# Performance work log

Hardware: AMD Instinct MI355X
Metric: run time of the kernel (lower is better)

The kernel has to match this reference:

```python
import jax, jax.numpy as jnp
import numpy as np

B, T, D = 8, 2048, 256
Q, K = 8, 1024


def setup_inputs() -> dict:
    key = jax.random.key(0)
    k1, k2 = jax.random.split(key)
    x = jax.random.normal(k1, (B, T, D), dtype=jnp.float32)
    codebooks = jax.random.normal(k2, (Q, K, D), dtype=jnp.float32)
    return {"x": x, "codebooks": codebooks}


def _vq_layer(residual, codebook):
    # residual: [B, T, D], codebook: [K, D]
    b, t, d = residual.shape
    flat = residual.reshape(-1, d)                      # [N, D]
    dist = (2.0 * flat @ codebook.T
            - jnp.sum(flat * flat, axis=-1, keepdims=True)
            - jnp.sum(codebook * codebook, axis=-1))    # [N, K]
    idx = jnp.argmax(dist, axis=-1)                     # [N]
    quantize = codebook[idx].reshape(b, t, d)           # gather
    # commitment loss (codebook updated via EMA in torch, not gradient)
    loss = jnp.mean((jax.lax.stop_gradient(quantize) - residual) ** 2)
    # straight-through estimator
    quantize_st = residual + jax.lax.stop_gradient(quantize - residual)
    return quantize_st, idx.reshape(b, t), loss


def reference(x, codebooks):
    def step(residual, codebook):
        q, idx, loss = _vq_layer(residual, codebook)
        return residual - q, (q, idx, loss)

    _, (qs, all_indices, all_losses) = jax.lax.scan(step, x, codebooks)
    quantized_out = jnp.sum(qs, axis=0)                 # [B, T, D]
    return quantized_out, all_indices, all_losses
```

## Files before the change

### kernel.cpp

```cpp
#include <hip/hip_runtime.h>


typedef _Float16 f16;
typedef f16 f16x8 __attribute__((ext_vector_type(8)));
typedef float f32x16 __attribute__((ext_vector_type(16)));

constexpr int Dd = 256;
constexpr int Kk = 1024;
constexpr int Qq = 8;
constexpr int Nn = 16384;

__device__ inline void gload16(const f16* g, f16* l) {
    __builtin_amdgcn_global_load_lds(
        (const __attribute__((address_space(1))) unsigned int*)(const __attribute__((address_space(1))) f16*)g,
        (__attribute__((address_space(3))) unsigned int*)(__attribute__((address_space(3))) f16*)l,
        16, 0, 0);
}

__global__ __launch_bounds__(256) void build_ecat(const float* __restrict__ cb,
                                                  f16* __restrict__ ecat,
                                                  float* __restrict__ norms) {
    int row = blockIdx.x * 8 + (threadIdx.x >> 5);
    int p = threadIdx.x & 31;
    const float* s = cb + (size_t)row * Dd + p * 8;
    f16x8 hi, lo;
    float sq = 0.f;
#pragma unroll
    for (int j = 0; j < 8; ++j) {
        float v = s[j];
        f16 h = (f16)v;
        hi[j] = h; lo[j] = (f16)(v - (float)h);
        sq = fmaf(v, v, sq);
    }
    *(f16x8*)(ecat + (size_t)row * 512 + p * 8) = hi;
    *(f16x8*)(ecat + (size_t)row * 512 + 256 + p * 8) = lo;
#pragma unroll
    for (int off = 16; off >= 1; off >>= 1) sq += __shfl_down(sq, off, 32);
    if (p == 0) norms[row] = sq;
}

__global__ __launch_bounds__(512, 2) void rvq_kernel(
    const float* __restrict__ x,
    const float* __restrict__ cbs,
    const f16* __restrict__ ecat,
    const float* __restrict__ norms,
    float* __restrict__ outq,
    float* __restrict__ idxs,
    float* __restrict__ losses)
{
    __shared__ f16 sA[2][16384];
    __shared__ f16 sB[32768];
    __shared__ float smn[1024];
    __shared__ float2 smg[4][64];
    __shared__ int bestk[64];
    __shared__ float lred[8];

    const int tid = threadIdx.x;
    const int w = tid >> 6, l = tid & 63;
    const int l32 = l & 31, lh = l >> 5;
    const int wcq = w >> 1;
    const int wt = w & 1;
    const int tbase = blockIdx.x * 64;
    const int ut = tid >> 3, ud = tid & 7;
    const int grow = tbase + ut;

    const int srow = tid >> 2;
    const int g = ((tid & 3) ^ ((tid >> 5) & 3)) * 8;

    int offA_[2][2];
#pragma unroll
    for (int m = 0; m < 2; ++m)
#pragma unroll
        for (int kh = 0; kh < 2; ++kh) {
            int row = wcq * 64 + m * 32 + l32;
            offA_[m][kh] = row * 32 + (((kh * 2 + lh) ^ ((row >> 3) & 3)) * 8);
        }
    int rbh[4][2];
#pragma unroll
    for (int cc = 0; cc < 4; ++cc)
#pragma unroll
        for (int kh = 0; kh < 2; ++kh) {
            int row = wt * 32 + l32;
            rbh[cc][kh] = row * 32 + ((((kh * 2 + lh) ^ ((row >> 3) & 3)) ^ cc) * 8);
        }

    float r[32];

#define STAGE(P, pp, c) do { \
        const f16* ga_ = gqs + (size_t)(pp) * 131072 + (c) * 32; \
        gload16(ga_,                  &sA[P][tid * 8]); \
        gload16(ga_ + 128 * 512,      &sA[P][4096 + tid * 8]); \
        gload16(ga_ + 256,            &sA[P][8192 + tid * 8]); \
        gload16(ga_ + 256 + 128 * 512,&sA[P][12288 + tid * 8]); \
    } while (0)

#pragma unroll 1
    for (int q = 0; q < Qq; ++q) {
        const f16* gqs = ecat + ((size_t)q * Kk + srow) * 512 + g;
        STAGE(0, 0, 0);
        STAGE(1, 0, 1);

        float lp = 0.f;
        if (q == 0) {
            const float4* xs = (const float4*)(x + (size_t)grow * Dd + ud * 32);
#pragma unroll
            for (int jv = 0; jv < 8; ++jv) {
                float4 v = xs[jv];
                r[jv * 4 + 0] = v.x; r[jv * 4 + 1] = v.y;
                r[jv * 4 + 2] = v.z; r[jv * 4 + 3] = v.w;
            }
        } else {
            const int k = bestk[ut];
            const float4* e4 = (const float4*)(cbs + ((size_t)(q - 1) * Kk + k) * Dd + ud * 32);
#pragma unroll
            for (int jv = 0; jv < 8; ++jv) {
                float4 v = e4[jv];
                r[jv * 4 + 0] -= v.x; r[jv * 4 + 1] -= v.y;
                r[jv * 4 + 2] -= v.z; r[jv * 4 + 3] -= v.w;
            }
#pragma unroll
            for (int j = 0; j < 32; ++j) lp = fmaf(r[j], r[j], lp);
            if ((tid & 7) == 0) idxs[(size_t)(q - 1) * Nn + grow] = (float)k;
#pragma unroll
            for (int off = 32; off >= 1; off >>= 1) lp += __shfl_down(lp, off);
            if (l == 0) lred[w] = lp;
        }
        {
            const int s = (ut >> 3) & 3;
#pragma unroll
            for (int qd = 0; qd < 4; ++qd) {
                f16x8 hi, lo;
#pragma unroll
                for (int j2 = 0; j2 < 8; ++j2) {
                    float v = 2.f * r[qd * 8 + j2];
                    f16 h = (f16)v;
                    hi[j2] = h; lo[j2] = (f16)(v - (float)h);
                }
                int a = ud * 2048 + ut * 32 + ((((qd ^ s) ^ (ud & 3)) & 3) * 8);
                *(f16x8*)&sB[a] = hi;
                *(f16x8*)&sB[16384 + a] = lo;
            }
        }
        smn[tid] = norms[q * Kk + tid];
        smn[512 + tid] = norms[q * Kk + 512 + tid];
        __syncthreads();
        if (q > 0 && tid == 0) {
            float s2 = 0.f;
#pragma unroll
            for (int i = 0; i < 8; ++i) s2 += lred[i];
            atomicAdd(losses + q - 1, s2 * (1.0f / ((float)Nn * (float)Dd)));
        }

        float bv = -3.4e38f; int bi = 0;
#pragma unroll 1
        for (int p = 0; p < 4; ++p) {
            f32x16 acc[2] = {};
#pragma unroll
            for (int c = 0; c < 8; ++c) {
                const int P = c & 1;
                if (c >= 1 && c < 7) STAGE(P ^ 1, p, c + 1);
#pragma unroll
                for (int kh = 0; kh < 2; ++kh) {
                    f16x8 a0 = *(const f16x8*)&sA[P][offA_[0][kh]];
                    f16x8 a1 = *(const f16x8*)&sA[P][offA_[1][kh]];
                    f16x8 bh = *(const f16x8*)&sB[c * 2048 + rbh[c & 3][kh]];
                    f16x8 bl = *(const f16x8*)&sB[16384 + c * 2048 + rbh[c & 3][kh]];
                    __builtin_amdgcn_s_setprio(1);
                    acc[0] = __builtin_amdgcn_mfma_f32_32x32x16_f16(a0, bh, acc[0], 0, 0, 0);
                    acc[1] = __builtin_amdgcn_mfma_f32_32x32x16_f16(a1, bh, acc[1], 0, 0, 0);
                    acc[0] = __builtin_amdgcn_mfma_f32_32x32x16_f16(a0, bl, acc[0], 0, 0, 0);
                    acc[1] = __builtin_amdgcn_mfma_f32_32x32x16_f16(a1, bl, acc[1], 0, 0, 0);
                    __builtin_amdgcn_s_setprio(0);
                    f16x8 e0 = *(const f16x8*)&sA[P][8192 + offA_[0][kh]];
                    f16x8 e1 = *(const f16x8*)&sA[P][8192 + offA_[1][kh]];
                    __builtin_amdgcn_s_setprio(1);
                    acc[0] = __builtin_amdgcn_mfma_f32_32x32x16_f16(e0, bh, acc[0], 0, 0, 0);
                    acc[1] = __builtin_amdgcn_mfma_f32_32x32x16_f16(e1, bh, acc[1], 0, 0, 0);
                    __builtin_amdgcn_s_setprio(0);
                }
                if (c < 7)
                    asm volatile("s_waitcnt vmcnt(0)\n\ts_barrier" ::: "memory");
            }
            asm volatile("s_barrier" ::: "memory");
            if (p < 3) { STAGE(0, p + 1, 0); STAGE(1, p + 1, 1); }
#pragma unroll
            for (int m = 0; m < 2; ++m) {
#pragma unroll
                for (int rr = 0; rr < 16; ++rr) {
                    int cl = wcq * 64 + m * 32 + (rr & 3) + 8 * (rr >> 2) + 4 * lh;
                    float v = acc[m][rr] - smn[p * 256 + cl];
                    int cg = p * 256 + cl;
                    if (v > bv) { bv = v; bi = cg; }
                }
            }
            if (p < 3)
                asm volatile("s_waitcnt vmcnt(4)\n\ts_barrier" ::: "memory");
        }
        {
            float ov = __shfl_xor(bv, 32);
            int oi = __shfl_xor(bi, 32);
            if (ov > bv || (ov == bv && oi < bi)) { bv = ov; bi = oi; }
            if (l < 32) smg[wcq][wt * 32 + l] = make_float2(bv, (float)bi);
            __syncthreads();
            if (tid < 64) {
                float2 r2 = smg[0][tid];
#pragma unroll
                for (int ww = 1; ww < 4; ++ww) {
                    float2 c2 = smg[ww][tid];
                    if (c2.x > r2.x || (c2.x == r2.x && c2.y < r2.y)) r2 = c2;
                }
                bestk[tid] = (int)r2.y;
            }
            __syncthreads();
        }
    }
#undef STAGE

    {
        const int k = bestk[ut];
        const float4* e4 = (const float4*)(cbs + ((size_t)7 * Kk + k) * Dd + ud * 32);
        float lp = 0.f;
#pragma unroll
        for (int jv = 0; jv < 8; ++jv) {
            float4 v = e4[jv];
            r[jv * 4 + 0] -= v.x; r[jv * 4 + 1] -= v.y;
            r[jv * 4 + 2] -= v.z; r[jv * 4 + 3] -= v.w;
        }
#pragma unroll
        for (int j = 0; j < 32; ++j) lp = fmaf(r[j], r[j], lp);
        const float4* xs = (const float4*)(x + (size_t)grow * Dd + ud * 32);
        float4* os = (float4*)(outq + (size_t)grow * Dd + ud * 32);
#pragma unroll
        for (int jv = 0; jv < 8; ++jv) {
            float4 xv = xs[jv];
            float4 o;
            o.x = xv.x - r[jv * 4 + 0]; o.y = xv.y - r[jv * 4 + 1];
            o.z = xv.z - r[jv * 4 + 2]; o.w = xv.w - r[jv * 4 + 3];
            os[jv] = o;
        }
        if ((tid & 7) == 0) idxs[(size_t)7 * Nn + grow] = (float)k;
#pragma unroll
        for (int off = 32; off >= 1; off >>= 1) lp += __shfl_down(lp, off);
        if (l == 0) lred[w] = lp;
        __syncthreads();
        if (tid == 0) {
            float s2 = 0.f;
#pragma unroll
            for (int i = 0; i < 8; ++i) s2 += lred[i];
            atomicAdd(losses + 7, s2 * (1.0f / ((float)Nn * (float)Dd)));
        }
    }
}

extern "C" void kernel_launch(void* const* d_in, const int* in_sizes, int n_in,
                              void* d_out, int out_size, void* d_ws, size_t ws_size,
                              hipStream_t stream) {
    const float* x   = (const float*)d_in[0];
    const float* cbs = (const float*)d_in[1];
    float* out    = (float*)d_out;
    float* idxs   = out + (size_t)Nn * Dd;
    float* losses = idxs + (size_t)Qq * Nn;

    f16* ecat    = (f16*)d_ws;
    float* norms = (float*)(ecat + (size_t)Qq * Kk * 512);

    hipMemsetAsync(losses, 0, Qq * sizeof(float), stream);
    build_ecat<<<(Qq * Kk) / 8, 256, 0, stream>>>(cbs, ecat, norms);
    rvq_kernel<<<Nn / 64, 512, 0, stream>>>(x, cbs, ecat, norms,
                                            out, idxs, losses);
}
```

Baseline: 284.8 us.

## Load codebook MFMA fragments directly from global into registers, drop LDS staging

Removes the double-buffered LDS staging of the fp16 hi/lo codebook tiles (global_load_lds plus per-chunk barriers). Each wave now reads its A fragments straight from global memory into registers, with a one-step register prefetch. This is meant to cut barrier synchronisation and LDS traffic and pressure. In exchange, codebook rows that were shared through LDS are now fetched by each wave separately, relying on L1/L2 caching. Global-load latency is now exposed, hidden only by a shallow prefetch.

New measurement: 518.7 us. 82.1% more time.

```diff
diff --git a/kernel.cpp b/kernel.cpp
--- a/kernel.cpp
+++ b/kernel.cpp
@@ -9,13 +9,6 @@
 constexpr int Kk = 1024;
 constexpr int Qq = 8;
 constexpr int Nn = 16384;
-
-__device__ inline void gload16(const f16* g, f16* l) {
-    __builtin_amdgcn_global_load_lds(
-        (const __attribute__((address_space(1))) unsigned int*)(const __attribute__((address_space(1))) f16*)g,
-        (__attribute__((address_space(3))) unsigned int*)(__attribute__((address_space(3))) f16*)l,
-        16, 0, 0);
-}
 
 __global__ __launch_bounds__(256) void build_ecat(const float* __restrict__ cb,
                                                   f16* __restrict__ ecat,
@@ -48,7 +41,6 @@
     float* __restrict__ idxs,
     float* __restrict__ losses)
 {
-    __shared__ f16 sA[2][16384];
     __shared__ f16 sB[32768];
     __shared__ float smn[1024];
     __shared__ float2 smg[4][64];
@@ -64,17 +56,6 @@
     const int ut = tid >> 3, ud = tid & 7;
     const int grow = tbase + ut;
 
-    const int srow = tid >> 2;
-    const int g = ((tid & 3) ^ ((tid >> 5) & 3)) * 8;
-
-    int offA_[2][2];
-#pragma unroll
-    for (int m = 0; m < 2; ++m)
-#pragma unroll
-        for (int kh = 0; kh < 2; ++kh) {
-            int row = wcq * 64 + m * 32 + l32;
-            offA_[m][kh] = row * 32 + (((kh * 2 + lh) ^ ((row >> 3) & 3)) * 8);
-        }
     int rbh[4][2];
 #pragma unroll
     for (int cc = 0; cc < 4; ++cc)
@@ -86,20 +67,8 @@
 
     float r[32];
 
-#define STAGE(P, pp, c) do { \
-        const f16* ga_ = gqs + (size_t)(pp) * 131072 + (c) * 32; \
-        gload16(ga_,                  &sA[P][tid * 8]); \
-        gload16(ga_ + 128 * 512,      &sA[P][4096 + tid * 8]); \
-        gload16(ga_ + 256,            &sA[P][8192 + tid * 8]); \
-        gload16(ga_ + 256 + 128 * 512,&sA[P][12288 + tid * 8]); \
-    } while (0)
-
 #pragma unroll 1
     for (int q = 0; q < Qq; ++q) {
-        const f16* gqs = ecat + ((size_t)q * Kk + srow) * 512 + g;
-        STAGE(0, 0, 0);
-        STAGE(1, 0, 1);
-
         float lp = 0.f;
         if (q == 0) {
             const float4* xs = (const float4*)(x + (size_t)grow * Dd + ud * 32);
@@ -154,35 +123,39 @@
         float bv = -3.4e38f; int bi = 0;
 #pragma unroll 1
         for (int p = 0; p < 4; ++p) {
+            const f16* a0p = ecat + ((size_t)q * Kk + p * 256 + wcq * 64 + l32) * 512 + lh * 8;
+            const f16* a1p = a0p + (size_t)32 * 512;
+
             f32x16 acc[2] = {};
-#pragma unroll
-            for (int c = 0; c < 8; ++c) {
-                const int P = c & 1;
-                if (c >= 1 && c < 7) STAGE(P ^ 1, p, c + 1);
-#pragma unroll
-                for (int kh = 0; kh < 2; ++kh) {
-                    f16x8 a0 = *(const f16x8*)&sA[P][offA_[0][kh]];
-                    f16x8 a1 = *(const f16x8*)&sA[P][offA_[1][kh]];
-                    f16x8 bh = *(const f16x8*)&sB[c * 2048 + rbh[c & 3][kh]];
-                    f16x8 bl = *(const f16x8*)&sB[16384 + c * 2048 + rbh[c & 3][kh]];
-                    __builtin_amdgcn_s_setprio(1);
-                    acc[0] = __builtin_amdgcn_mfma_f32_32x32x16_f16(a0, bh, acc[0], 0, 0, 0);
-                    acc[1] = __builtin_amdgcn_mfma_f32_32x32x16_f16(a1, bh, acc[1], 0, 0, 0);
-                    acc[0] = __builtin_amdgcn_mfma_f32_32x32x16_f16(a0, bl, acc[0], 0, 0, 0);
-                    acc[1] = __builtin_amdgcn_mfma_f32_32x32x16_f16(a1, bl, acc[1], 0, 0, 0);
-                    __builtin_amdgcn_s_setprio(0);
-                    f16x8 e0 = *(const f16x8*)&sA[P][8192 + offA_[0][kh]];
-                    f16x8 e1 = *(const f16x8*)&sA[P][8192 + offA_[1][kh]];
-                    __builtin_amdgcn_s_setprio(1);
-                    acc[0] = __builtin_amdgcn_mfma_f32_32x32x16_f16(e0, bh, acc[0], 0, 0, 0);
-                    acc[1] = __builtin_amdgcn_mfma_f32_32x32x16_f16(e1, bh, acc[1], 0, 0, 0);
-                    __builtin_amdgcn_s_setprio(0);
-                }
-                if (c < 7)
-                    asm volatile("s_waitcnt vmcnt(0)\n\ts_barrier" ::: "memory");
-            }
-            asm volatile("s_barrier" ::: "memory");
-            if (p < 3) { STAGE(0, p + 1, 0); STAGE(1, p + 1, 1); }
+            f16x8 fa0[2], fa1[2], fe0[2], fe1[2], fbh[2], fbl[2];
+
+#define LOADF(S, IDX) do { \
+            const int c_ = (IDX) >> 1, kh_ = (IDX) & 1; \
+            const int co_ = c_ * 32 + kh_ * 16; \
+            fa0[S] = *(const f16x8*)(a0p + co_); \
+            fa1[S] = *(const f16x8*)(a1p + co_); \
+            fe0[S] = *(const f16x8*)(a0p + 256 + co_); \
+            fe1[S] = *(const f16x8*)(a1p + 256 + co_); \
+            fbh[S] = *(const f16x8*)&sB[c_ * 2048 + rbh[c_ & 3][kh_]]; \
+            fbl[S] = *(const f16x8*)&sB[16384 + c_ * 2048 + rbh[c_ & 3][kh_]]; \
+        } while (0)
+
+            LOADF(0, 0);
+#pragma unroll
+            for (int idx = 0; idx < 16; ++idx) {
+                const int cur = idx & 1;
+                if (idx < 15) LOADF(cur ^ 1, idx + 1);
+                __builtin_amdgcn_s_setprio(1);
+                acc[0] = __builtin_amdgcn_mfma_f32_32x32x16_f16(fa0[cur], fbh[cur], acc[0], 0, 0, 0);
+                acc[1] = __builtin_amdgcn_mfma_f32_32x32x16_f16(fa1[cur], fbh[cur], acc[1], 0, 0, 0);
+                acc[0] = __builtin_amdgcn_mfma_f32_32x32x16_f16(fa0[cur], fbl[cur], acc[0], 0, 0, 0);
+                acc[1] = __builtin_amdgcn_mfma_f32_32x32x16_f16(fa1[cur], fbl[cur], acc[1], 0, 0, 0);
+                acc[0] = __builtin_amdgcn_mfma_f32_32x32x16_f16(fe0[cur], fbh[cur], acc[0], 0, 0, 0);
+                acc[1] = __builtin_amdgcn_mfma_f32_32x32x16_f16(fe1[cur], fbh[cur], acc[1], 0, 0, 0);
+                __builtin_amdgcn_s_setprio(0);
+            }
+#undef LOADF
+
 #pragma unroll
             for (int m = 0; m < 2; ++m) {
 #pragma unroll
@@ -193,8 +166,6 @@
                     if (v > bv) { bv = v; bi = cg; }
                 }
             }
-            if (p < 3)
-                asm volatile("s_waitcnt vmcnt(4)\n\ts_barrier" ::: "memory");
         }
         {
             float ov = __shfl_xor(bv, 32);
@@ -214,7 +185,6 @@
             __syncthreads();
         }
     }
-#undef STAGE
 
     {
         const int k = bestk[ut];
```

## Double block to 1024 threads covering 512 codewords per pass with finer K-chunk staging

Applied to the files above, without the earlier changes.

The RVQ kernel now launches 1024 threads (16 waves) per block, so each pass covers 512 codebook rows instead of 256 and two passes replace four. The A-tile staging is restructured into 16 half-chunks of 16 columns with one hi/lo load pair per thread, and double-buffering runs continuously across the pass boundary. Each thread holds 16 residual elements instead of 32, which lowers register pressure. The aim is more waves in flight to hide load latency and fewer pass-boundary stalls, at the cost of a barrier every half-chunk across 16 waves and a launch bound that may force register spills.

Result: slower. 334.4 us (+17.4%).

```diff
diff --git a/kernel.cpp b/kernel.cpp
--- a/kernel.cpp
+++ b/kernel.cpp
@@ -39,7 +39,7 @@
     if (p == 0) norms[row] = sq;
 }
 
-__global__ __launch_bounds__(512, 2) void rvq_kernel(
+__global__ __launch_bounds__(1024, 4) void rvq_kernel(
     const float* __restrict__ x,
     const float* __restrict__ cbs,
     const f16* __restrict__ ecat,
@@ -51,30 +51,25 @@
     __shared__ f16 sA[2][16384];
     __shared__ f16 sB[32768];
     __shared__ float smn[1024];
-    __shared__ float2 smg[4][64];
+    __shared__ float2 smg[8][64];
     __shared__ int bestk[64];
-    __shared__ float lred[8];
+    __shared__ float lred[16];
 
     const int tid = threadIdx.x;
     const int w = tid >> 6, l = tid & 63;
     const int l32 = l & 31, lh = l >> 5;
-    const int wcq = w >> 1;
+    const int cs = w >> 1;
     const int wt = w & 1;
     const int tbase = blockIdx.x * 64;
-    const int ut = tid >> 3, ud = tid & 7;
+    const int ut = tid >> 4, h = tid & 15;
     const int grow = tbase + ut;
 
-    const int srow = tid >> 2;
-    const int g = ((tid & 3) ^ ((tid >> 5) & 3)) * 8;
-
-    int offA_[2][2];
-#pragma unroll
-    for (int m = 0; m < 2; ++m)
-#pragma unroll
-        for (int kh = 0; kh < 2; ++kh) {
-            int row = wcq * 64 + m * 32 + l32;
-            offA_[m][kh] = row * 32 + (((kh * 2 + lh) ^ ((row >> 3) & 3)) * 8);
-        }
+    int offA[2];
+#pragma unroll
+    for (int m = 0; m < 2; ++m) {
+        int ra = cs * 64 + m * 32 + l32;
+        offA[m] = ra * 16 + ((lh ^ ((ra >> 2) & 1)) * 8);
+    }
     int rbh[4][2];
 #pragma unroll
     for (int cc = 0; cc < 4; ++cc)
@@ -84,128 +79,120 @@
             rbh[cc][kh] = row * 32 + ((((kh * 2 + lh) ^ ((row >> 3) & 3)) ^ cc) * 8);
         }
 
-    float r[32];
-
-#define STAGE(P, pp, c) do { \
-        const f16* ga_ = gqs + (size_t)(pp) * 131072 + (c) * 32; \
-        gload16(ga_,                  &sA[P][tid * 8]); \
-        gload16(ga_ + 128 * 512,      &sA[P][4096 + tid * 8]); \
-        gload16(ga_ + 256,            &sA[P][8192 + tid * 8]); \
-        gload16(ga_ + 256 + 128 * 512,&sA[P][12288 + tid * 8]); \
+    const int ch8 = (((tid & 1) ^ ((tid >> 3) & 1))) * 8;
+
+    float r[16];
+
+#define STAGE(P, PP, HC) do { \
+        const f16* ga_ = ecat + ((size_t)q * Kk + (PP) * 512 + (tid >> 1)) * 512 + (HC) * 16 + ch8; \
+        gload16(ga_,       &sA[P][tid * 8]); \
+        gload16(ga_ + 256, &sA[P][8192 + tid * 8]); \
     } while (0)
 
 #pragma unroll 1
     for (int q = 0; q < Qq; ++q) {
-        const f16* gqs = ecat + ((size_t)q * Kk + srow) * 512 + g;
         STAGE(0, 0, 0);
-        STAGE(1, 0, 1);
 
         float lp = 0.f;
         if (q == 0) {
-            const float4* xs = (const float4*)(x + (size_t)grow * Dd + ud * 32);
-#pragma unroll
-            for (int jv = 0; jv < 8; ++jv) {
+            const float4* xs = (const float4*)(x + (size_t)grow * Dd + h * 16);
+#pragma unroll
+            for (int jv = 0; jv < 4; ++jv) {
                 float4 v = xs[jv];
                 r[jv * 4 + 0] = v.x; r[jv * 4 + 1] = v.y;
                 r[jv * 4 + 2] = v.z; r[jv * 4 + 3] = v.w;
             }
         } else {
             const int k = bestk[ut];
-            const float4* e4 = (const float4*)(cbs + ((size_t)(q - 1) * Kk + k) * Dd + ud * 32);
-#pragma unroll
-            for (int jv = 0; jv < 8; ++jv) {
+            const float4* e4 = (const float4*)(cbs + ((size_t)(q - 1) * Kk + k) * Dd + h * 16);
+#pragma unroll
+            for (int jv = 0; jv < 4; ++jv) {
                 float4 v = e4[jv];
                 r[jv * 4 + 0] -= v.x; r[jv * 4 + 1] -= v.y;
                 r[jv * 4 + 2] -= v.z; r[jv * 4 + 3] -= v.w;
             }
 #pragma unroll
-            for (int j = 0; j < 32; ++j) lp = fmaf(r[j], r[j], lp);
-            if ((tid & 7) == 0) idxs[(size_t)(q - 1) * Nn + grow] = (float)k;
+            for (int j = 0; j < 16; ++j) lp = fmaf(r[j], r[j], lp);
+            if (h == 0) idxs[(size_t)(q - 1) * Nn + grow] = (float)k;
 #pragma unroll
             for (int off = 32; off >= 1; off >>= 1) lp += __shfl_down(lp, off);
             if (l == 0) lred[w] = lp;
         }
         {
             const int s = (ut >> 3) & 3;
-#pragma unroll
-            for (int qd = 0; qd < 4; ++qd) {
+            const int st = h >> 1;
+#pragma unroll
+            for (int j = 0; j < 2; ++j) {
+                const int qq = (h & 1) * 2 + j;
                 f16x8 hi, lo;
 #pragma unroll
                 for (int j2 = 0; j2 < 8; ++j2) {
-                    float v = 2.f * r[qd * 8 + j2];
-                    f16 h = (f16)v;
-                    hi[j2] = h; lo[j2] = (f16)(v - (float)h);
+                    float v = 2.f * r[j * 8 + j2];
+                    f16 hv = (f16)v;
+                    hi[j2] = hv; lo[j2] = (f16)(v - (float)hv);
                 }
-                int a = ud * 2048 + ut * 32 + ((((qd ^ s) ^ (ud & 3)) & 3) * 8);
+                int a = st * 2048 + ut * 32 + (((qq ^ s) ^ (st & 3)) & 3) * 8;
                 *(f16x8*)&sB[a] = hi;
                 *(f16x8*)&sB[16384 + a] = lo;
             }
         }
         smn[tid] = norms[q * Kk + tid];
-        smn[512 + tid] = norms[q * Kk + 512 + tid];
         __syncthreads();
         if (q > 0 && tid == 0) {
             float s2 = 0.f;
 #pragma unroll
-            for (int i = 0; i < 8; ++i) s2 += lred[i];
+            for (int i = 0; i < 16; ++i) s2 += lred[i];
             atomicAdd(losses + q - 1, s2 * (1.0f / ((float)Nn * (float)Dd)));
         }
 
         float bv = -3.4e38f; int bi = 0;
 #pragma unroll 1
-        for (int p = 0; p < 4; ++p) {
+        for (int p = 0; p < 2; ++p) {
             f32x16 acc[2] = {};
 #pragma unroll
-            for (int c = 0; c < 8; ++c) {
-                const int P = c & 1;
-                if (c >= 1 && c < 7) STAGE(P ^ 1, p, c + 1);
-#pragma unroll
-                for (int kh = 0; kh < 2; ++kh) {
-                    f16x8 a0 = *(const f16x8*)&sA[P][offA_[0][kh]];
-                    f16x8 a1 = *(const f16x8*)&sA[P][offA_[1][kh]];
-                    f16x8 bh = *(const f16x8*)&sB[c * 2048 + rbh[c & 3][kh]];
-                    f16x8 bl = *(const f16x8*)&sB[16384 + c * 2048 + rbh[c & 3][kh]];
-                    __builtin_amdgcn_s_setprio(1);
-                    acc[0] = __builtin_amdgcn_mfma_f32_32x32x16_f16(a0, bh, acc[0], 0, 0, 0);
-                    acc[1] = __builtin_amdgcn_mfma_f32_32x32x16_f16(a1, bh, acc[1], 0, 0, 0);
-                    acc[0] = __builtin_amdgcn_mfma_f32_32x32x16_f16(a0, bl, acc[0], 0, 0, 0);
-                    acc[1] = __builtin_amdgcn_mfma_f32_32x32x16_f16(a1, bl, acc[1], 0, 0, 0);
-                    __builtin_amdgcn_s_setprio(0);
-                    f16x8 e0 = *(const f16x8*)&sA[P][8192 + offA_[0][kh]];
-                    f16x8 e1 = *(const f16x8*)&sA[P][8192 + offA_[1][kh]];
-                    __builtin_amdgcn_s_setprio(1);
-                    acc[0] = __builtin_amdgcn_mfma_f32_32x32x16_f16(e0, bh, acc[0], 0, 0, 0);
-                    acc[1] = __builtin_amdgcn_mfma_f32_32x32x16_f16(e1, bh, acc[1], 0, 0, 0);
-                    __builtin_amdgcn_s_setprio(0);
-                }
-                if (c < 7)
+            for (int hc = 0; hc < 16; ++hc) {
+                const int P = hc & 1;
+                if (hc < 15)            STAGE(P ^ 1, p, hc + 1);
+                else if (p == 0)        STAGE(P ^ 1, 1, 0);
+                const int c = hc >> 1, kh = hc & 1;
+                f16x8 a0 = *(const f16x8*)&sA[P][offA[0]];
+                f16x8 a1 = *(const f16x8*)&sA[P][offA[1]];
+                f16x8 bh = *(const f16x8*)&sB[c * 2048 + rbh[c & 3][kh]];
+                f16x8 bl = *(const f16x8*)&sB[16384 + c * 2048 + rbh[c & 3][kh]];
+                f16x8 e0 = *(const f16x8*)&sA[P][8192 + offA[0]];
+                f16x8 e1 = *(const f16x8*)&sA[P][8192 + offA[1]];
+                __builtin_amdgcn_s_setprio(1);
+                acc[0] = __builtin_amdgcn_mfma_f32_32x32x16_f16(a0, bh, acc[0], 0, 0, 0);
+                acc[1] = __builtin_amdgcn_mfma_f32_32x32x16_f16(a1, bh, acc[1], 0, 0, 0);
+                acc[0] = __builtin_amdgcn_mfma_f32_32x32x16_f16(a0, bl, acc[0], 0, 0, 0);
+                acc[1] = __builtin_amdgcn_mfma_f32_32x32x16_f16(a1, bl, acc[1], 0, 0, 0);
+                acc[0] = __builtin_amdgcn_mfma_f32_32x32x16_f16(e0, bh, acc[0], 0, 0, 0);
+                acc[1] = __builtin_amdgcn_mfma_f32_32x32x16_f16(e1, bh, acc[1], 0, 0, 0);
+                __builtin_amdgcn_s_setprio(0);
+                if (p * 16 + hc < 31)
                     asm volatile("s_waitcnt vmcnt(0)\n\ts_barrier" ::: "memory");
             }
-            asm volatile("s_barrier" ::: "memory");
-            if (p < 3) { STAGE(0, p + 1, 0); STAGE(1, p + 1, 1); }
 #pragma unroll
             for (int m = 0; m < 2; ++m) {
 #pragma unroll
                 for (int rr = 0; rr < 16; ++rr) {
-                    int cl = wcq * 64 + m * 32 + (rr & 3) + 8 * (rr >> 2) + 4 * lh;
-                    float v = acc[m][rr] - smn[p * 256 + cl];
-                    int cg = p * 256 + cl;
+                    int cl = cs * 64 + m * 32 + (rr & 3) + 8 * (rr >> 2) + 4 * lh;
+                    int cg = p * 512 + cl;
+                    float v = acc[m][rr] - smn[cg];
                     if (v > bv) { bv = v; bi = cg; }
                 }
             }
-            if (p < 3)
-                asm volatile("s_waitcnt vmcnt(4)\n\ts_barrier" ::: "memory");
         }
         {
             float ov = __shfl_xor(bv, 32);
             int oi = __shfl_xor(bi, 32);
             if (ov > bv || (ov == bv && oi < bi)) { bv = ov; bi = oi; }
-            if (l < 32) smg[wcq][wt * 32 + l] = make_float2(bv, (float)bi);
+            if (l < 32) smg[cs][wt * 32 + l32] = make_float2(bv, (float)bi);
             __syncthreads();
             if (tid < 64) {
                 float2 r2 = smg[0][tid];
 #pragma unroll
-                for (int ww = 1; ww < 4; ++ww) {
+                for (int ww = 1; ww < 8; ++ww) {
                     float2 c2 = smg[ww][tid];
                     if (c2.x > r2.x || (c2.x == r2.x && c2.y < r2.y)) r2 = c2;
                 }
@@ -218,27 +205,27 @@
 
     {
         const int k = bestk[ut];
-        const float4* e4 = (const float4*)(cbs + ((size_t)7 * Kk + k) * Dd + ud * 32);
+        const float4* e4 = (const float4*)(cbs + ((size_t)7 * Kk + k) * Dd + h * 16);
         float lp = 0.f;
 #pragma unroll
-        for (int jv = 0; jv < 8; ++jv) {
+        for (int jv = 0; jv < 4; ++jv) {
             float4 v = e4[jv];
             r[jv * 4 + 0] -= v.x; r[jv * 4 + 1] -= v.y;
             r[jv * 4 + 2] -= v.z; r[jv * 4 + 3] -= v.w;
         }
 #pragma unroll
-        for (int j = 0; j < 32; ++j) lp = fmaf(r[j], r[j], lp);
-        const float4* xs = (const float4*)(x + (size_t)grow * Dd + ud * 32);
-        float4* os = (float4*)(outq + (size_t)grow * Dd + ud * 32);
-#pragma unroll
-        for (int jv = 0; jv < 8; ++jv) {
+        for (int j = 0; j < 16; ++j) lp = fmaf(r[j], r[j], lp);
+        const float4* xs = (const float4*)(x + (size_t)grow * Dd + h * 16);
+        float4* os = (float4*)(outq + (size_t)grow * Dd + h * 16);
+#pragma unroll
+        for (int jv = 0; jv < 4; ++jv) {
             float4 xv = xs[jv];
             float4 o;
             o.x = xv.x - r[jv * 4 + 0]; o.y = xv.y - r[jv * 4 + 1];
             o.z = xv.z - r[jv * 4 + 2]; o.w = xv.w - r[jv * 4 + 3];
             os[jv] = o;
         }
-        if ((tid & 7) == 0) idxs[(size_t)7 * Nn + grow] = (float)k;
+        if (h == 0) idxs[(size_t)7 * Nn + grow] = (float)k;
 #pragma unroll
         for (int off = 32; off >= 1; off >>= 1) lp += __shfl_down(lp, off);
         if (l == 0) lred[w] = lp;
@@ -246,7 +233,7 @@
         if (tid == 0) {
             float s2 = 0.f;
 #pragma unroll
-            for (int i = 0; i < 8; ++i) s2 += lred[i];
+            for (int i = 0; i < 16; ++i) s2 += lred[i];
             atomicAdd(losses + 7, s2 * (1.0f / ((float)Nn * (float)Dd)));
         }
     }
@@ -266,6 +253,6 @@
 
     hipMemsetAsync(losses, 0, Qq * sizeof(float), stream);
     build_ecat<<<(Qq * Kk) / 8, 256, 0, stream>>>(cbs, ecat, norms);
-    rvq_kernel<<<Nn / 64, 512, 0, stream>>>(x, cbs, ecat, norms,
-                                            out, idxs, losses);
-}
+    rvq_kernel<<<Nn / 64, 1024, 0, stream>>>(x, cbs, ecat, norms,
+                                             out, idxs, losses);
+}
```
